# Optimization experiments

Hardware: AMD Instinct MI355X
Metric: run time of the kernel (lower is better)

The kernel has to match this reference:

```python
import jax, jax.numpy as jnp
import numpy as np

V, D, T, L, H = 32000, 1024, 2048, 2, 16
HS = D // H  # per-head dim (head_size // nheads)
FF = 4 * D
EPS = 1e-5


def _ln(x, g, b):
    m = jnp.mean(x, axis=-1, keepdims=True)
    v = jnp.mean((x - m) ** 2, axis=-1, keepdims=True)
    return (x - m) * jax.lax.rsqrt(v + EPS) * g + b


def setup_inputs() -> dict:
    key = jax.random.key(0)
    ks = jax.random.split(key, 16)
    s = lambda k, shape, fan: jax.random.normal(k, shape, jnp.float32) * (fan ** -0.5)
    return {
        "inputs": jax.random.randint(ks[0], (1, T), 0, V, dtype=jnp.int64),
        "tok_emb": s(ks[1], (V, D), D),
        "pos_emb": s(ks[2], (T, D), D),
        "ln1_g": jnp.ones((L, D)), "ln1_b": jnp.zeros((L, D)),
        "wq": s(ks[3], (L, H, D, HS), D),
        "wk": s(ks[4], (L, H, D, HS), D),
        "wv": s(ks[5], (L, H, D, HS), D),
        "ln2_g": jnp.ones((L, D)), "ln2_b": jnp.zeros((L, D)),
        "w1": s(ks[6], (L, D, FF), D), "b1": jnp.zeros((L, FF)),
        "w2": s(ks[7], (L, FF, D), FF), "b2": jnp.zeros((L, D)),
        "lnf_g": jnp.ones((D,)), "lnf_b": jnp.zeros((D,)),
        "w_un": s(ks[8], (D, V), D), "b_un": jnp.zeros((V,)),
    }


def reference(inputs, tok_emb, pos_emb, ln1_g, ln1_b, wq, wk, wv,
              ln2_g, ln2_b, w1, b1, w2, b2, lnf_g, lnf_b, w_un, b_un):
    b, t = inputs.shape
    x = tok_emb[inputs] + pos_emb[:t]  # [B,T,D]
    mask = jnp.tril(jnp.ones((t, t), dtype=bool))
    scale = jnp.asarray(D, x.dtype) ** -0.5  # source scales by x.shape[-1]**-0.5
    neg_inf = jnp.asarray(-jnp.inf, x.dtype)
    for l in range(L):
        h = _ln(x, ln1_g[l], ln1_b[l])
        q = jnp.einsum('btc,hcs->bhts', h, wq[l])
        k = jnp.einsum('btc,hcs->bhts', h, wk[l])
        v = jnp.einsum('btc,hcs->bhts', h, wv[l])
        scores = jnp.einsum('bhts,bhus->bhtu', q, k) * scale  # [B,H,T,T]
        scores = jnp.where(mask, scores, neg_inf)
        p = jax.nn.softmax(scores, axis=-1)
        att = jnp.einsum('bhtu,bhus->bhts', p, v)  # [B,H,T,HS]
        att = att.transpose(0, 2, 1, 3).reshape(b, t, H * HS)
        x = x + att
        h = _ln(x, ln2_g[l], ln2_b[l])
        h = jax.nn.relu(h @ w1[l] + b1[l]) @ w2[l] + b2[l]
        x = x + h
    x = _ln(x, lnf_g, lnf_b)
    return x @ w_un + b_un  # [B,T,V]
```

## Files before the change

### kernel.cpp

```cpp
#include <hip/hip_runtime.h>
#include <hip/hip_bf16.h>

#define TT 2048
#define DD 1024
#define NH 16
#define HSZ 64
#define FFD 4096
#define VV 32000
#define NL 2

typedef __bf16 bf16x8 __attribute__((ext_vector_type(8)));
typedef float f32x4 __attribute__((ext_vector_type(4)));

__device__ __forceinline__ unsigned short f2bf(float f) {
    unsigned int u = __float_as_uint(f);
    return (unsigned short)((u + 0x7FFFu + ((u >> 16) & 1u)) >> 16);
}

#define GLL(gsrc, ldst) \
  __builtin_amdgcn_global_load_lds((const __attribute__((address_space(1))) void*)(gsrc), \
                                   (__attribute__((address_space(3))) void*)(ldst), 16, 0, 0)

#define SWZ64(L)  ((L) ^ ((((L) >> 7) & 3) << 4))
#define SWZ128(L) ((L) ^ ((((L) >> 7) & 7) << 4))

__global__ __launch_bounds__(256) void embed_kernel(
    const int* __restrict__ idx, const float* __restrict__ tok,
    const float* __restrict__ pos, float* __restrict__ x)
{
    int t = blockIdx.x;
    int d4 = threadIdx.x * 4;
    int token = idx[t];
    float4 a = *(const float4*)&tok[(size_t)token * DD + d4];
    float4 p = *(const float4*)&pos[(size_t)t * DD + d4];
    float4 r;
    r.x = a.x + p.x; r.y = a.y + p.y; r.z = a.z + p.z; r.w = a.w + p.w;
    *(float4*)&x[(size_t)t * DD + d4] = r;
}

__global__ __launch_bounds__(256) void ln_kernel(
    const float* __restrict__ x, const float* __restrict__ g,
    const float* __restrict__ b, unsigned short* __restrict__ out)
{
    int t = blockIdx.x;
    int tid = threadIdx.x;
    int d4 = tid * 4;
    float4 xv = *(const float4*)&x[(size_t)t * DD + d4];
    float s  = xv.x + xv.y + xv.z + xv.w;
    float s2 = xv.x*xv.x + xv.y*xv.y + xv.z*xv.z + xv.w*xv.w;
    #pragma unroll
    for (int off = 32; off >= 1; off >>= 1) {
        s  += __shfl_xor(s,  off);
        s2 += __shfl_xor(s2, off);
    }
    __shared__ float ls[4], ls2[4];
    int w = tid >> 6;
    if ((tid & 63) == 0) { ls[w] = s; ls2[w] = s2; }
    __syncthreads();
    float sum  = ls[0] + ls[1] + ls[2] + ls[3];
    float sum2 = ls2[0] + ls2[1] + ls2[2] + ls2[3];
    float mean = sum * (1.0f / DD);
    float var  = sum2 * (1.0f / DD) - mean * mean;
    float r = rsqrtf(var + 1e-5f);
    float4 gv = *(const float4*)&g[d4];
    float4 bv = *(const float4*)&b[d4];
    ushort4 pk;
    pk.x = f2bf((xv.x - mean) * r * gv.x + bv.x);
    pk.y = f2bf((xv.y - mean) * r * gv.y + bv.y);
    pk.z = f2bf((xv.z - mean) * r * gv.z + bv.z);
    pk.w = f2bf((xv.w - mean) * r * gv.w + bv.w);
    *(ushort4*)&out[(size_t)t * DD + d4] = pk;
}

__global__ __launch_bounds__(256) void tcast(
    const float* __restrict__ src, unsigned short* __restrict__ dst,
    int R, int C, size_t sstride, size_t dstride)
{
    __shared__ float tile[64][65];
    const float* s = src + (size_t)blockIdx.z * sstride;
    unsigned short* d = dst + (size_t)blockIdx.z * dstride;
    int c0 = blockIdx.x * 64, r0 = blockIdx.y * 64;
    #pragma unroll
    for (int i = 0; i < 16; ++i) {
        int id = i * 256 + threadIdx.x;
        int rr = id >> 6, cc = id & 63;
        tile[rr][cc] = s[(size_t)(r0 + rr) * C + (c0 + cc)];
    }
    __syncthreads();
    #pragma unroll
    for (int i = 0; i < 16; ++i) {
        int id = i * 256 + threadIdx.x;
        int cc = id >> 6, rr = id & 63;
        d[(size_t)(c0 + cc) * R + (r0 + rr)] = f2bf(tile[rr][cc]);
    }
}

__global__ __launch_bounds__(256) void qkv_tcast(
    const float* __restrict__ wq, const float* __restrict__ wk,
    const float* __restrict__ wv, unsigned short* __restrict__ dst)
{
    __shared__ float tile[64][65];
    int l = blockIdx.z;
    int mat = blockIdx.y >> 4, hh = blockIdx.y & 15;
    const float* s = (mat == 0) ? wq : (mat == 1) ? wk : wv;
    s += (((size_t)l * NH + hh) * DD) * HSZ;
    int r0 = blockIdx.x * 64;
    #pragma unroll
    for (int i = 0; i < 16; ++i) {
        int id = i * 256 + threadIdx.x;
        int rr = id >> 6, cc = id & 63;
        tile[rr][cc] = s[(size_t)(r0 + rr) * HSZ + cc];
    }
    __syncthreads();
    unsigned short* d = dst + (size_t)l * 3072 * DD + ((size_t)mat * DD + hh * HSZ) * DD;
    #pragma unroll
    for (int i = 0; i < 16; ++i) {
        int id = i * 256 + threadIdx.x;
        int cc = id >> 6, rr = id & 63;
        d[(size_t)cc * DD + (r0 + rr)] = f2bf(tile[rr][cc]);
    }
}

template<int EPI>
__global__ __launch_bounds__(256) void mgemm(
    const unsigned short* __restrict__ A, const unsigned short* __restrict__ Bt,
    const float* __restrict__ bias, void* __restrict__ outp,
    int M, int N, int K)
{
    __shared__ unsigned short As[2][128 * 32];
    __shared__ unsigned short Bs[2][128 * 32];
    int tid = threadIdx.x;
    int w = tid >> 6, lane = tid & 63;
    int l15 = lane & 15, l4 = lane >> 4;
    int bm = blockIdx.y * 128, bn = blockIdx.x * 128;
    int wr = (w >> 1) * 64, wc = (w & 1) * 64;

    f32x4 zz = {0.f, 0.f, 0.f, 0.f};
    f32x4 acc[4][4];
    #pragma unroll
    for (int m = 0; m < 4; ++m)
        #pragma unroll
        for (int n = 0; n < 4; ++n) acc[m][n] = zz;

    int t16 = tid * 16;
    int lg = SWZ64(t16);
    int srow = lg >> 6;
    int skel = (lg & 63) >> 1;
    const unsigned short* aS0 = A + (size_t)(bm + srow) * K + skel;
    const unsigned short* aS1 = A + (size_t)(bm + 64 + srow) * K + skel;
    const unsigned short* bS0 = Bt + (size_t)(bn + srow) * K + skel;
    const unsigned short* bS1 = Bt + (size_t)(bn + 64 + srow) * K + skel;

    #define STAGE(t, buf) do { int kk_ = (t) * 32; \
        GLL(aS0 + kk_, (char*)As[buf] + w * 1024); \
        GLL(aS1 + kk_, (char*)As[buf] + 4096 + w * 1024); \
        GLL(bS0 + kk_, (char*)Bs[buf] + w * 1024); \
        GLL(bS1 + kk_, (char*)Bs[buf] + 4096 + w * 1024); } while (0)

    int aoff[4], boff[4];
    #pragma unroll
    for (int m = 0; m < 4; ++m) {
        int la = (wr + m * 16 + l15) * 64 + l4 * 16;
        aoff[m] = SWZ64(la);
        int lb = (wc + m * 16 + l15) * 64 + l4 * 16;
        boff[m] = SWZ64(lb);
    }

    int nt = K >> 5;
    STAGE(0, 0);
    STAGE(1, 1);
    for (int t = 0; t < nt; ++t) {
        int buf = t & 1;
        if (t + 1 < nt) asm volatile("s_waitcnt vmcnt(4)" ::: "memory");
        else            asm volatile("s_waitcnt vmcnt(0)" ::: "memory");
        __builtin_amdgcn_sched_barrier(0);
        __builtin_amdgcn_s_barrier();
        __builtin_amdgcn_sched_barrier(0);
        bf16x8 af[4], bfr[4];
        #pragma unroll
        for (int m = 0; m < 4; ++m) af[m] = *(const bf16x8*)((const char*)As[buf] + aoff[m]);
        #pragma unroll
        for (int n = 0; n < 4; ++n) bfr[n] = *(const bf16x8*)((const char*)Bs[buf] + boff[n]);
        #pragma unroll
        for (int m = 0; m < 4; ++m)
            #pragma unroll
            for (int n = 0; n < 4; ++n)
                acc[m][n] = __builtin_amdgcn_mfma_f32_16x16x32_bf16(af[m], bfr[n], acc[m][n], 0, 0, 0);
        __builtin_amdgcn_sched_barrier(0);
        __builtin_amdgcn_s_barrier();
        __builtin_amdgcn_sched_barrier(0);
        if (t + 2 < nt) STAGE(t + 2, buf);
    }
    #undef STAGE

    #pragma unroll
    for (int m = 0; m < 4; ++m) {
        int row0 = bm + wr + m * 16 + l4 * 4;
        #pragma unroll
        for (int n = 0; n < 4; ++n) {
            int col = bn + wc + n * 16 + l15;
            f32x4 v = acc[m][n];
            if (EPI == 0) {
                int mat = col >> 10, hh = (col >> 6) & 15, ss = col & 63;
                unsigned short* base = (unsigned short*)outp + (size_t)mat * ((size_t)NH * TT * HSZ);
                if (mat < 2) {
                    #pragma unroll
                    for (int i = 0; i < 4; ++i)
                        base[((size_t)hh * TT + row0 + i) * HSZ + ss] = f2bf(v[i]);
                } else {
                    ushort4 pk;
                    pk.x = f2bf(v[0]); pk.y = f2bf(v[1]); pk.z = f2bf(v[2]); pk.w = f2bf(v[3]);
                    *(ushort4*)&base[((size_t)hh * HSZ + ss) * TT + row0] = pk;
                }
            } else if (EPI == 1) {
                float bb = bias[col];
                unsigned short* o = (unsigned short*)outp;
                #pragma unroll
                for (int i = 0; i < 4; ++i)
                    o[(size_t)(row0 + i) * FFD + col] = f2bf(fmaxf(v[i] + bb, 0.f));
            } else if (EPI == 2) {
                float bb = bias[col];
                float* xx = (float*)outp;
                #pragma unroll
                for (int i = 0; i < 4; ++i)
                    xx[(size_t)(row0 + i) * DD + col] += v[i] + bb;
            }
        }
    }
}

__global__ __launch_bounds__(512, 2) void mgemm256(
    const unsigned short* __restrict__ A, const unsigned short* __restrict__ Bt,
    const float* __restrict__ bias, float* __restrict__ outp,
    int M, int N, int K)
{
    __shared__ unsigned short As[2][2][128 * 64];
    __shared__ unsigned short Bs[2][2][128 * 64];
    int tid = threadIdx.x;
    int w = tid >> 6, lane = tid & 63;
    int l15 = lane & 15, l4 = lane >> 4;
    int wr = w >> 2, wc = w & 3;
    int bid = blockIdx.x;
    int xcd = bid & 7, j = bid >> 3;
    int mt = j & 7, p = xcd * 16 + (j >> 3);
    if (p >= N / 256) return;
    int bm = mt * 256, bn = p * 256;

    f32x4 zz = {0.f, 0.f, 0.f, 0.f};
    f32x4 acc[8][4];
    #pragma unroll
    for (int m = 0; m < 8; ++m)
        #pragma unroll
        for (int n = 0; n < 4; ++n) acc[m][n] = zz;

    int L0 = w * 1024 + lane * 16;
    int Ls = SWZ128(L0);
    int srow = Ls >> 7;
    int skel = (Ls & 127) >> 1;
    const unsigned short* aS[2], *bS[2];
    aS[0] = A + (size_t)(bm + srow) * K + skel;
    aS[1] = A + (size_t)(bm + 128 + srow) * K + skel;
    bS[0] = Bt + (size_t)(bn + srow) * K + skel;
    bS[1] = Bt + (size_t)(bn + 128 + srow) * K + skel;
    size_t g1 = (size_t)64 * K;

    #define STAGE6(t, buf) do { int kk_ = (t) * 64; \
        GLL(aS[0] + kk_,      (char*)As[buf][0] + w * 1024); \
        GLL(aS[0] + g1 + kk_, (char*)As[buf][0] + 8192 + w * 1024); \
        GLL(aS[1] + kk_,      (char*)As[buf][1] + w * 1024); \
        GLL(aS[1] + g1 + kk_, (char*)As[buf][1] + 8192 + w * 1024); \
        GLL(bS[0] + kk_,      (char*)Bs[buf][0] + w * 1024); \
        GLL(bS[0] + g1 + kk_, (char*)Bs[buf][0] + 8192 + w * 1024); \
        GLL(bS[1] + kk_,      (char*)Bs[buf][1] + w * 1024); \
        GLL(bS[1] + g1 + kk_, (char*)Bs[buf][1] + 8192 + w * 1024); } while (0)

    int aoff[8][2], boff[4][2];
    #pragma unroll
    for (int m = 0; m < 8; ++m)
        #pragma unroll
        for (int ks = 0; ks < 2; ++ks) {
            int La = (m * 16 + l15) * 128 + ks * 64 + l4 * 16;
            aoff[m][ks] = SWZ128(La);
        }
    #pragma unroll
    for (int n = 0; n < 4; ++n)
        #pragma unroll
        for (int ks = 0; ks < 2; ++ks) {
            int Lb = ((wc & 1) * 64 + n * 16 + l15) * 128 + ks * 64 + l4 * 16;
            boff[n][ks] = SWZ128(Lb);
        }

    int nt = K >> 6;
    STAGE6(0, 0);
    STAGE6(1, 1);
    for (int t = 0; t < nt; ++t) {
        int buf = t & 1;
        if (t + 1 < nt) asm volatile("s_waitcnt vmcnt(8)" ::: "memory");
        else            asm volatile("s_waitcnt vmcnt(0)" ::: "memory");
        __builtin_amdgcn_sched_barrier(0);
        __builtin_amdgcn_s_barrier();
        __builtin_amdgcn_sched_barrier(0);
        const char* ab = (const char*)As[buf][wr];
        const char* bb = (const char*)Bs[buf][wc >> 1];
        bf16x8 bfr[4][2];
        #pragma unroll
        for (int n = 0; n < 4; ++n)
            #pragma unroll
            for (int ks = 0; ks < 2; ++ks)
                bfr[n][ks] = *(const bf16x8*)(bb + boff[n][ks]);
        __builtin_amdgcn_s_setprio(1);
        #pragma unroll
        for (int rh = 0; rh < 2; ++rh) {
            bf16x8 af[4][2];
            #pragma unroll
            for (int mm = 0; mm < 4; ++mm)
                #pragma unroll
                for (int ks = 0; ks < 2; ++ks)
                    af[mm][ks] = *(const bf16x8*)(ab + aoff[rh * 4 + mm][ks]);
            #pragma unroll
            for (int mm = 0; mm < 4; ++mm)
                #pragma unroll
                for (int n = 0; n < 4; ++n) {
                    acc[rh*4+mm][n] = __builtin_amdgcn_mfma_f32_16x16x32_bf16(af[mm][0], bfr[n][0], acc[rh*4+mm][n], 0, 0, 0);
                    acc[rh*4+mm][n] = __builtin_amdgcn_mfma_f32_16x16x32_bf16(af[mm][1], bfr[n][1], acc[rh*4+mm][n], 0, 0, 0);
                }
        }
        __builtin_amdgcn_s_setprio(0);
        __builtin_amdgcn_sched_barrier(0);
        __builtin_amdgcn_s_barrier();
        __builtin_amdgcn_sched_barrier(0);
        if (t + 2 < nt) STAGE6(t + 2, buf);
    }
    #undef STAGE6

    #pragma unroll
    for (int m = 0; m < 8; ++m) {
        int row0 = bm + wr * 128 + m * 16 + l4 * 4;
        #pragma unroll
        for (int n = 0; n < 4; ++n) {
            int col = bn + wc * 64 + n * 16 + l15;
            float bb = bias[col];
            f32x4 v = acc[m][n];
            #pragma unroll
            for (int i = 0; i < 4; ++i)
                outp[(size_t)(row0 + i) * VV + col] = v[i] + bb;
        }
    }
}

__global__ __launch_bounds__(256) void attn_kernel(
    const unsigned short* __restrict__ qg, const unsigned short* __restrict__ kg,
    const unsigned short* __restrict__ vt, float* __restrict__ x)
{
    __shared__ unsigned short Ks[2][64 * 64];
    __shared__ unsigned short Vs[2][64 * 64];
    __shared__ unsigned short Ps[4][16 * 64];
    int tid = threadIdx.x;
    int w = tid >> 6, lane = tid & 63;
    int l15 = lane & 15, l4 = lane >> 4;
    int hh = blockIdx.y;
    int qb = blockIdx.x * 64;

    const unsigned short* qrow = qg + ((size_t)hh * TT + qb + w * 16 + l15) * HSZ + l4 * 8;
    bf16x8 qf0 = *(const bf16x8*)(qrow);
    bf16x8 qf1 = *(const bf16x8*)(qrow + 32);

    int t16 = tid * 16;
    int lgs = SWZ128(t16);
    int surow = lgs >> 7;
    int subyte = lgs & 127;
    const char* kbase = (const char*)(kg + (size_t)hh * TT * HSZ);
    const char* vbase = (const char*)(vt + (size_t)hh * HSZ * TT);

    #define ASTAGE(ib, buf) do { \
        int ub_ = (ib) * 64; \
        GLL(kbase + (size_t)(ub_ + surow) * 128 + subyte,          (char*)Ks[buf] + w * 1024); \
        GLL(kbase + (size_t)(ub_ + 32 + surow) * 128 + subyte,     (char*)Ks[buf] + 4096 + w * 1024); \
        GLL(vbase + (size_t)surow * 4096 + ub_ * 2 + subyte,       (char*)Vs[buf] + w * 1024); \
        GLL(vbase + (size_t)(surow + 32) * 4096 + ub_ * 2 + subyte,(char*)Vs[buf] + 4096 + w * 1024); \
    } while (0)

    f32x4 zz = {0.f, 0.f, 0.f, 0.f};
    f32x4 o[4];
    #pragma unroll
    for (int i = 0; i < 4; ++i) o[i] = zz;
    float mrun = -INFINITY, lrun = 0.f;

    const float scale = 0.03125f;
    int nkv = (qb >> 6) + 1;
    ASTAGE(0, 0);
    __syncthreads();
    int cur = 0;
    for (int ib = 0; ib < nkv; ++ib) {
        int ub = ib * 64;
        bool diag = (ub == qb);
        if (ib + 1 < nkv) ASTAGE(ib + 1, cur ^ 1);
        const char* ksc = (const char*)Ks[cur];
        const char* vsc = (const char*)Vs[cur];

        f32x4 sfr[4];
        __builtin_amdgcn_s_setprio(1);
        #pragma unroll
        for (int f = 0; f < 4; ++f) {
            int lgb = (f * 16 + l15) * 128 + l4 * 16;
            bf16x8 k0 = *(const bf16x8*)(ksc + SWZ128(lgb));
            bf16x8 k1 = *(const bf16x8*)(ksc + SWZ128(lgb + 64));
            f32x4 z = zz;
            z = __builtin_amdgcn_mfma_f32_16x16x32_bf16(k0, qf0, z, 0, 0, 0);
            z = __builtin_amdgcn_mfma_f32_16x16x32_bf16(k1, qf1, z, 0, 0, 0);
            sfr[f] = z;
        }
        __builtin_amdgcn_s_setprio(0);

        float mx = -INFINITY;
        #pragma unroll
        for (int f = 0; f < 4; ++f)
            #pragma unroll
            for (int i = 0; i < 4; ++i) {
                float s = sfr[f][i] * scale;
                if (diag && (16 * f + (l4 << 2) + i) > (w * 16 + l15)) s = -INFINITY;
                sfr[f][i] = s;
                mx = fmaxf(mx, s);
            }
        mx = fmaxf(mx, __shfl_xor(mx, 16));
        mx = fmaxf(mx, __shfl_xor(mx, 32));
        float mn = fmaxf(mrun, mx);
        float c = __expf(mrun - mn);
        mrun = mn;
        float ps = 0.f;
        #pragma unroll
        for (int f = 0; f < 4; ++f)
            #pragma unroll
            for (int i = 0; i < 4; ++i) {
                float p = __expf(sfr[f][i] - mn);
                sfr[f][i] = p;
                ps += p;
            }
        ps += __shfl_xor(ps, 16);
        ps += __shfl_xor(ps, 32);
        lrun = lrun * c + ps;
        #pragma unroll
        for (int i = 0; i < 4; ++i) {
            float ci = __shfl(c, (lane & 48) + (l4 << 2) + i);
            #pragma unroll
            for (int sf = 0; sf < 4; ++sf) o[sf][i] *= ci;
        }

        unsigned short* pw = Ps[w];
        #pragma unroll
        for (int f = 0; f < 4; ++f) {
            unsigned a0 = ((unsigned)f2bf(sfr[f][0])) | (((unsigned)f2bf(sfr[f][1])) << 16);
            unsigned a1 = ((unsigned)f2bf(sfr[f][2])) | (((unsigned)f2bf(sfr[f][3])) << 16);
            int byte0 = l15 * 128 + (16 * f + (l4 << 2)) * 2;
            *(unsigned*)((char*)pw + SWZ128(byte0)) = a0;
            *(unsigned*)((char*)pw + SWZ128(byte0 + 4)) = a1;
        }
        bf16x8 pa0 = *(const bf16x8*)((const char*)pw + SWZ128(l15 * 128 + l4 * 16));
        bf16x8 pa1 = *(const bf16x8*)((const char*)pw + SWZ128(l15 * 128 + 64 + l4 * 16));
        __builtin_amdgcn_s_setprio(1);
        #pragma unroll
        for (int sf = 0; sf < 4; ++sf) {
            int lgb = (sf * 16 + l15) * 128 + l4 * 16;
            bf16x8 v0 = *(const bf16x8*)(vsc + SWZ128(lgb));
            bf16x8 v1 = *(const bf16x8*)(vsc + SWZ128(lgb + 64));
            o[sf] = __builtin_amdgcn_mfma_f32_16x16x32_bf16(pa0, v0, o[sf], 0, 0, 0);
            o[sf] = __builtin_amdgcn_mfma_f32_16x16x32_bf16(pa1, v1, o[sf], 0, 0, 0);
        }
        __builtin_amdgcn_s_setprio(0);
        __syncthreads();
        cur ^= 1;
    }
    #undef ASTAGE
    float rl[4];
    #pragma unroll
    for (int i = 0; i < 4; ++i)
        rl[i] = 1.0f / __shfl(lrun, (lane & 48) + (l4 << 2) + i);
    #pragma unroll
    for (int sf = 0; sf < 4; ++sf)
        #pragma unroll
        for (int i = 0; i < 4; ++i) {
            int q = qb + w * 16 + l4 * 4 + i;
            int d = hh * HSZ + sf * 16 + l15;
            x[(size_t)q * DD + d] += o[sf][i] * rl[i];
        }
}

extern "C" void kernel_launch(void* const* d_in, const int* in_sizes, int n_in,
                              void* d_out, int out_size, void* d_ws, size_t ws_size,
                              hipStream_t stream)
{
    const int*   idx    = (const int*)  d_in[0];
    const float* tok    = (const float*)d_in[1];
    const float* pos    = (const float*)d_in[2];
    const float* ln1_g  = (const float*)d_in[3];
    const float* ln1_b  = (const float*)d_in[4];
    const float* wq     = (const float*)d_in[5];
    const float* wk     = (const float*)d_in[6];
    const float* wv     = (const float*)d_in[7];
    const float* ln2_g  = (const float*)d_in[8];
    const float* ln2_b  = (const float*)d_in[9];
    const float* w1     = (const float*)d_in[10];
    const float* b1     = (const float*)d_in[11];
    const float* w2     = (const float*)d_in[12];
    const float* b2     = (const float*)d_in[13];
    const float* lnf_g  = (const float*)d_in[14];
    const float* lnf_b  = (const float*)d_in[15];
    const float* w_un   = (const float*)d_in[16];
    const float* b_un   = (const float*)d_in[17];
    float* out = (float*)d_out;

    char* W = (char*)d_ws;
    float*          x    = (float*)(W);
    unsigned short* h    = (unsigned short*)(W + 8388608);
    unsigned short* qg   = (unsigned short*)(W + 12582912);
    unsigned short* kg   = (unsigned short*)(W + 16777216);
    unsigned short* vt   = (unsigned short*)(W + 20971520);
    unsigned short* h1   = (unsigned short*)(W + 25165824);
    unsigned short* wqkvT= (unsigned short*)(W + 41943040);
    unsigned short* w1T  = (unsigned short*)(W + 54525952);
    unsigned short* w2T  = (unsigned short*)(W + 71303168);
    unsigned short* wunT = (unsigned short*)(W + 88080384);
    (void)kg; (void)ws_size; (void)in_sizes; (void)n_in; (void)out_size;

    qkv_tcast<<<dim3(16, 48, 2), 256, 0, stream>>>(wq, wk, wv, wqkvT);
    tcast<<<dim3(64, 16, 2), 256, 0, stream>>>(w1, w1T, DD, FFD, (size_t)DD * FFD, (size_t)DD * FFD);
    tcast<<<dim3(16, 64, 2), 256, 0, stream>>>(w2, w2T, FFD, DD, (size_t)FFD * DD, (size_t)FFD * DD);
    tcast<<<dim3(500, 16, 1), 256, 0, stream>>>(w_un, wunT, DD, VV, 0, 0);

    embed_kernel<<<TT, 256, 0, stream>>>(idx, tok, pos, x);

    for (int l = 0; l < NL; ++l) {
        ln_kernel<<<TT, 256, 0, stream>>>(x, ln1_g + l * DD, ln1_b + l * DD, h);
        mgemm<0><<<dim3(24, 16), 256, 0, stream>>>(h, wqkvT + (size_t)l * 3072 * DD, nullptr, qg, TT, 3072, DD);
        attn_kernel<<<dim3(32, 16), 256, 0, stream>>>(qg, kg, vt, x);
        ln_kernel<<<TT, 256, 0, stream>>>(x, ln2_g + l * DD, ln2_b + l * DD, h);
        mgemm<1><<<dim3(32, 16), 256, 0, stream>>>(h, w1T + (size_t)l * FFD * DD, b1 + (size_t)l * FFD, h1, TT, FFD, DD);
        mgemm<2><<<dim3(8, 16), 256, 0, stream>>>(h1, w2T + (size_t)l * DD * FFD, b2 + (size_t)l * DD, x, TT, DD, FFD);
    }

    ln_kernel<<<TT, 256, 0, stream>>>(x, lnf_g, lnf_b, h);
    mgemm256<<<dim3(1024), 512, 0, stream>>>(h, wunT, b_un, out, TT, VV, DD);
}
```

Measured before the change: 702.2 us.

## Triple-buffer GEMM loads, prefetch attention KV deeper, add lazy softmax rescale

Result: slower. 717.7 us (+2.2%).

```diff
diff --git a/kernel.cpp b/kernel.cpp
--- a/kernel.cpp
+++ b/kernel.cpp
@@ -127,8 +127,8 @@
     const float* __restrict__ bias, void* __restrict__ outp,
     int M, int N, int K)
 {
-    __shared__ unsigned short As[2][128 * 32];
-    __shared__ unsigned short Bs[2][128 * 32];
+    __shared__ unsigned short As[3][128 * 32];
+    __shared__ unsigned short Bs[3][128 * 32];
     int tid = threadIdx.x;
     int w = tid >> 6, lane = tid & 63;
     int l15 = lane & 15, l4 = lane >> 4;
@@ -151,11 +151,11 @@
     const unsigned short* bS0 = Bt + (size_t)(bn + srow) * K + skel;
     const unsigned short* bS1 = Bt + (size_t)(bn + 64 + srow) * K + skel;
 
-    #define STAGE(t, buf) do { int kk_ = (t) * 32; \
-        GLL(aS0 + kk_, (char*)As[buf] + w * 1024); \
-        GLL(aS1 + kk_, (char*)As[buf] + 4096 + w * 1024); \
-        GLL(bS0 + kk_, (char*)Bs[buf] + w * 1024); \
-        GLL(bS1 + kk_, (char*)Bs[buf] + 4096 + w * 1024); } while (0)
+    #define STAGE(t, slot) do { int kk_ = (t) * 32; \
+        GLL(aS0 + kk_, (char*)As[slot] + w * 1024); \
+        GLL(aS1 + kk_, (char*)As[slot] + 4096 + w * 1024); \
+        GLL(bS0 + kk_, (char*)Bs[slot] + w * 1024); \
+        GLL(bS1 + kk_, (char*)Bs[slot] + 4096 + w * 1024); } while (0)
 
     int aoff[4], boff[4];
     #pragma unroll
@@ -169,18 +169,20 @@
     int nt = K >> 5;
     STAGE(0, 0);
     STAGE(1, 1);
+    STAGE(2, 2);
+    int slot = 0;
     for (int t = 0; t < nt; ++t) {
-        int buf = t & 1;
-        if (t + 1 < nt) asm volatile("s_waitcnt vmcnt(4)" ::: "memory");
-        else            asm volatile("s_waitcnt vmcnt(0)" ::: "memory");
+        if (t + 2 < nt)      asm volatile("s_waitcnt vmcnt(8)" ::: "memory");
+        else if (t + 1 < nt) asm volatile("s_waitcnt vmcnt(4)" ::: "memory");
+        else                 asm volatile("s_waitcnt vmcnt(0)" ::: "memory");
         __builtin_amdgcn_sched_barrier(0);
         __builtin_amdgcn_s_barrier();
         __builtin_amdgcn_sched_barrier(0);
         bf16x8 af[4], bfr[4];
         #pragma unroll
-        for (int m = 0; m < 4; ++m) af[m] = *(const bf16x8*)((const char*)As[buf] + aoff[m]);
-        #pragma unroll
-        for (int n = 0; n < 4; ++n) bfr[n] = *(const bf16x8*)((const char*)Bs[buf] + boff[n]);
+        for (int m = 0; m < 4; ++m) af[m] = *(const bf16x8*)((const char*)As[slot] + aoff[m]);
+        #pragma unroll
+        for (int n = 0; n < 4; ++n) bfr[n] = *(const bf16x8*)((const char*)Bs[slot] + boff[n]);
         #pragma unroll
         for (int m = 0; m < 4; ++m)
             #pragma unroll
@@ -189,7 +191,8 @@
         __builtin_amdgcn_sched_barrier(0);
         __builtin_amdgcn_s_barrier();
         __builtin_amdgcn_sched_barrier(0);
-        if (t + 2 < nt) STAGE(t + 2, buf);
+        if (t + 3 < nt) STAGE(t + 3, slot);
+        slot = (slot == 2) ? 0 : slot + 1;
     }
     #undef STAGE
 
@@ -234,8 +237,8 @@
     const float* __restrict__ bias, float* __restrict__ outp,
     int M, int N, int K)
 {
-    __shared__ unsigned short As[2][2][128 * 64];
-    __shared__ unsigned short Bs[2][2][128 * 64];
+    __shared__ unsigned short As[3][2][128 * 32];
+    __shared__ unsigned short Bs[3][2][128 * 32];
     int tid = threadIdx.x;
     int w = tid >> 6, lane = tid & 63;
     int l15 = lane & 15, l4 = lane >> 4;
@@ -253,83 +256,61 @@
         #pragma unroll
         for (int n = 0; n < 4; ++n) acc[m][n] = zz;
 
-    int L0 = w * 1024 + lane * 16;
-    int Ls = SWZ128(L0);
-    int srow = Ls >> 7;
-    int skel = (Ls & 127) >> 1;
+    int L0 = tid * 16;
+    int Ls = SWZ64(L0);
+    int srow = Ls >> 6;
+    int skel = (Ls & 63) >> 1;
     const unsigned short* aS[2], *bS[2];
     aS[0] = A + (size_t)(bm + srow) * K + skel;
     aS[1] = A + (size_t)(bm + 128 + srow) * K + skel;
     bS[0] = Bt + (size_t)(bn + srow) * K + skel;
     bS[1] = Bt + (size_t)(bn + 128 + srow) * K + skel;
-    size_t g1 = (size_t)64 * K;
-
-    #define STAGE6(t, buf) do { int kk_ = (t) * 64; \
-        GLL(aS[0] + kk_,      (char*)As[buf][0] + w * 1024); \
-        GLL(aS[0] + g1 + kk_, (char*)As[buf][0] + 8192 + w * 1024); \
-        GLL(aS[1] + kk_,      (char*)As[buf][1] + w * 1024); \
-        GLL(aS[1] + g1 + kk_, (char*)As[buf][1] + 8192 + w * 1024); \
-        GLL(bS[0] + kk_,      (char*)Bs[buf][0] + w * 1024); \
-        GLL(bS[0] + g1 + kk_, (char*)Bs[buf][0] + 8192 + w * 1024); \
-        GLL(bS[1] + kk_,      (char*)Bs[buf][1] + w * 1024); \
-        GLL(bS[1] + g1 + kk_, (char*)Bs[buf][1] + 8192 + w * 1024); } while (0)
-
-    int aoff[8][2], boff[4][2];
+
+    #define STAGE6(t, slot) do { int kk_ = (t) * 32; \
+        GLL(aS[0] + kk_, (char*)As[slot][0] + w * 1024); \
+        GLL(aS[1] + kk_, (char*)As[slot][1] + w * 1024); \
+        GLL(bS[0] + kk_, (char*)Bs[slot][0] + w * 1024); \
+        GLL(bS[1] + kk_, (char*)Bs[slot][1] + w * 1024); } while (0)
+
+    int aoff[8], boff[4];
     #pragma unroll
     for (int m = 0; m < 8; ++m)
-        #pragma unroll
-        for (int ks = 0; ks < 2; ++ks) {
-            int La = (m * 16 + l15) * 128 + ks * 64 + l4 * 16;
-            aoff[m][ks] = SWZ128(La);
-        }
+        aoff[m] = SWZ64((m * 16 + l15) * 64 + l4 * 16);
     #pragma unroll
     for (int n = 0; n < 4; ++n)
-        #pragma unroll
-        for (int ks = 0; ks < 2; ++ks) {
-            int Lb = ((wc & 1) * 64 + n * 16 + l15) * 128 + ks * 64 + l4 * 16;
-            boff[n][ks] = SWZ128(Lb);
-        }
-
-    int nt = K >> 6;
+        boff[n] = SWZ64(((wc & 1) * 64 + n * 16 + l15) * 64 + l4 * 16);
+
+    int nt = K >> 5;
     STAGE6(0, 0);
     STAGE6(1, 1);
+    STAGE6(2, 2);
+    int slot = 0;
     for (int t = 0; t < nt; ++t) {
-        int buf = t & 1;
-        if (t + 1 < nt) asm volatile("s_waitcnt vmcnt(8)" ::: "memory");
-        else            asm volatile("s_waitcnt vmcnt(0)" ::: "memory");
+        if (t + 2 < nt)      asm volatile("s_waitcnt vmcnt(8)" ::: "memory");
+        else if (t + 1 < nt) asm volatile("s_waitcnt vmcnt(4)" ::: "memory");
+        else                 asm volatile("s_waitcnt vmcnt(0)" ::: "memory");
         __builtin_amdgcn_sched_barrier(0);
         __builtin_amdgcn_s_barrier();
         __builtin_amdgcn_sched_barrier(0);
-        const char* ab = (const char*)As[buf][wr];
-        const char* bb = (const char*)Bs[buf][wc >> 1];
-        bf16x8 bfr[4][2];
-        #pragma unroll
-        for (int n = 0; n < 4; ++n)
+        const char* ab = (const char*)As[slot][wr];
+        const char* bb = (const char*)Bs[slot][wc >> 1];
+        bf16x8 bfr[4];
+        #pragma unroll
+        for (int n = 0; n < 4; ++n) bfr[n] = *(const bf16x8*)(bb + boff[n]);
+        __builtin_amdgcn_s_setprio(1);
+        #pragma unroll
+        for (int m = 0; m < 8; ++m) {
+            bf16x8 af = *(const bf16x8*)(ab + aoff[m]);
             #pragma unroll
-            for (int ks = 0; ks < 2; ++ks)
-                bfr[n][ks] = *(const bf16x8*)(bb + boff[n][ks]);
-        __builtin_amdgcn_s_setprio(1);
-        #pragma unroll
-        for (int rh = 0; rh < 2; ++rh) {
-            bf16x8 af[4][2];
-            #pragma unroll
-            for (int mm = 0; mm < 4; ++mm)
-                #pragma unroll
-                for (int ks = 0; ks < 2; ++ks)
-                    af[mm][ks] = *(const bf16x8*)(ab + aoff[rh * 4 + mm][ks]);
-            #pragma unroll
-            for (int mm = 0; mm < 4; ++mm)
-                #pragma unroll
-                for (int n = 0; n < 4; ++n) {
-                    acc[rh*4+mm][n] = __builtin_amdgcn_mfma_f32_16x16x32_bf16(af[mm][0], bfr[n][0], acc[rh*4+mm][n], 0, 0, 0);
-                    acc[rh*4+mm][n] = __builtin_amdgcn_mfma_f32_16x16x32_bf16(af[mm][1], bfr[n][1], acc[rh*4+mm][n], 0, 0, 0);
-                }
+            for (int n = 0; n < 4; ++n)
+                acc[m][n] = __builtin_amdgcn_mfma_f32_16x16x32_bf16(af, bfr[n], acc[m][n], 0, 0, 0);
         }
         __builtin_amdgcn_s_setprio(0);
         __builtin_amdgcn_sched_barrier(0);
         __builtin_amdgcn_s_barrier();
         __builtin_amdgcn_sched_barrier(0);
-        if (t + 2 < nt) STAGE6(t + 2, buf);
+        if (t + 3 < nt) STAGE6(t + 3, slot);
+        slot = (slot == 2) ? 0 : slot + 1;
     }
     #undef STAGE6
 
@@ -359,7 +340,7 @@
     int w = tid >> 6, lane = tid & 63;
     int l15 = lane & 15, l4 = lane >> 4;
     int hh = blockIdx.y;
-    int qb = blockIdx.x * 64;
+    int qb = (31 - blockIdx.x) * 64;
 
     const unsigned short* qrow = qg + ((size_t)hh * TT + qb + w * 16 + l15) * HSZ + l4 * 8;
     bf16x8 qf0 = *(const bf16x8*)(qrow);
@@ -389,12 +370,15 @@
     const float scale = 0.03125f;
     int nkv = (qb >> 6) + 1;
     ASTAGE(0, 0);
-    __syncthreads();
+    if (nkv > 1) ASTAGE(1, 1);
     int cur = 0;
     for (int ib = 0; ib < nkv; ++ib) {
-        int ub = ib * 64;
-        bool diag = (ub == qb);
-        if (ib + 1 < nkv) ASTAGE(ib + 1, cur ^ 1);
+        bool diag = (ib * 64 == qb);
+        if (ib + 1 < nkv) asm volatile("s_waitcnt vmcnt(4)" ::: "memory");
+        else              asm volatile("s_waitcnt vmcnt(0)" ::: "memory");
+        __builtin_amdgcn_sched_barrier(0);
+        __builtin_amdgcn_s_barrier();
+        __builtin_amdgcn_sched_barrier(0);
         const char* ksc = (const char*)Ks[cur];
         const char* vsc = (const char*)Vs[cur];
 
@@ -424,26 +408,32 @@
             }
         mx = fmaxf(mx, __shfl_xor(mx, 16));
         mx = fmaxf(mx, __shfl_xor(mx, 32));
-        float mn = fmaxf(mrun, mx);
-        float c = __expf(mrun - mn);
-        mrun = mn;
+        bool grow = __any(mx > mrun + 8.0f);
+        float c = 1.0f;
+        if (grow) {
+            float mn = fmaxf(mrun, mx);
+            c = __expf(mrun - mn);
+            mrun = mn;
+        }
         float ps = 0.f;
         #pragma unroll
         for (int f = 0; f < 4; ++f)
             #pragma unroll
             for (int i = 0; i < 4; ++i) {
-                float p = __expf(sfr[f][i] - mn);
+                float p = __expf(sfr[f][i] - mrun);
                 sfr[f][i] = p;
                 ps += p;
             }
         ps += __shfl_xor(ps, 16);
         ps += __shfl_xor(ps, 32);
         lrun = lrun * c + ps;
-        #pragma unroll
-        for (int i = 0; i < 4; ++i) {
-            float ci = __shfl(c, (lane & 48) + (l4 << 2) + i);
+        if (grow) {
             #pragma unroll
-            for (int sf = 0; sf < 4; ++sf) o[sf][i] *= ci;
+            for (int i = 0; i < 4; ++i) {
+                float ci = __shfl(c, (lane & 48) + (l4 << 2) + i);
+                #pragma unroll
+                for (int sf = 0; sf < 4; ++sf) o[sf][i] *= ci;
+            }
         }
 
         unsigned short* pw = Ps[w];
@@ -467,7 +457,10 @@
             o[sf] = __builtin_amdgcn_mfma_f32_16x16x32_bf16(pa1, v1, o[sf], 0, 0, 0);
         }
         __builtin_amdgcn_s_setprio(0);
-        __syncthreads();
+        __builtin_amdgcn_sched_barrier(0);
+        __builtin_amdgcn_s_barrier();
+        __builtin_amdgcn_sched_barrier(0);
+        if (ib + 2 < nkv) ASTAGE(ib + 2, cur);
         cur ^= 1;
     }
     #undef ASTAGE
```

## Triple-buffer GEMM, add BN=64 tiles, reverse attention order, lazy softmax rescale

Applied to the files above, without the earlier changes.

After: 658.9 us. -6.2%, faster.

```diff
diff --git a/kernel.cpp b/kernel.cpp
--- a/kernel.cpp
+++ b/kernel.cpp
@@ -23,6 +23,8 @@
 
 #define SWZ64(L)  ((L) ^ ((((L) >> 7) & 3) << 4))
 #define SWZ128(L) ((L) ^ ((((L) >> 7) & 7) << 4))
+
+#define VMW(n) asm volatile("s_waitcnt vmcnt(" #n ")" ::: "memory")
 
 __global__ __launch_bounds__(256) void embed_kernel(
     const int* __restrict__ idx, const float* __restrict__ tok,
@@ -121,26 +123,27 @@
     }
 }
 
-template<int EPI>
+template<int EPI, int BN>
 __global__ __launch_bounds__(256) void mgemm(
     const unsigned short* __restrict__ A, const unsigned short* __restrict__ Bt,
     const float* __restrict__ bias, void* __restrict__ outp,
     int M, int N, int K)
 {
-    __shared__ unsigned short As[2][128 * 32];
-    __shared__ unsigned short Bs[2][128 * 32];
+    constexpr int FN = BN / 64 * 2;
+    __shared__ unsigned short As[3][128 * 32];
+    __shared__ unsigned short Bs[3][BN * 32];
     int tid = threadIdx.x;
     int w = tid >> 6, lane = tid & 63;
     int l15 = lane & 15, l4 = lane >> 4;
-    int bm = blockIdx.y * 128, bn = blockIdx.x * 128;
-    int wr = (w >> 1) * 64, wc = (w & 1) * 64;
+    int bm = blockIdx.y * 128, bn = blockIdx.x * BN;
+    int wr = (w >> 1) * 64, wc = (w & 1) * (BN / 2);
 
     f32x4 zz = {0.f, 0.f, 0.f, 0.f};
-    f32x4 acc[4][4];
+    f32x4 acc[4][FN];
     #pragma unroll
     for (int m = 0; m < 4; ++m)
         #pragma unroll
-        for (int n = 0; n < 4; ++n) acc[m][n] = zz;
+        for (int n = 0; n < FN; ++n) acc[m][n] = zz;
 
     int t16 = tid * 16;
     int lg = SWZ64(t16);
@@ -151,45 +154,53 @@
     const unsigned short* bS0 = Bt + (size_t)(bn + srow) * K + skel;
     const unsigned short* bS1 = Bt + (size_t)(bn + 64 + srow) * K + skel;
 
-    #define STAGE(t, buf) do { int kk_ = (t) * 32; \
-        GLL(aS0 + kk_, (char*)As[buf] + w * 1024); \
-        GLL(aS1 + kk_, (char*)As[buf] + 4096 + w * 1024); \
-        GLL(bS0 + kk_, (char*)Bs[buf] + w * 1024); \
-        GLL(bS1 + kk_, (char*)Bs[buf] + 4096 + w * 1024); } while (0)
-
-    int aoff[4], boff[4];
-    #pragma unroll
-    for (int m = 0; m < 4; ++m) {
-        int la = (wr + m * 16 + l15) * 64 + l4 * 16;
-        aoff[m] = SWZ64(la);
-        int lb = (wc + m * 16 + l15) * 64 + l4 * 16;
-        boff[m] = SWZ64(lb);
-    }
+    #define STAGE(t, slot) do { int kk_ = (t) * 32; \
+        GLL(aS0 + kk_, (char*)As[slot] + w * 1024); \
+        GLL(aS1 + kk_, (char*)As[slot] + 4096 + w * 1024); \
+        GLL(bS0 + kk_, (char*)Bs[slot] + w * 1024); \
+        if (BN == 128) GLL(bS1 + kk_, (char*)Bs[slot] + 4096 + w * 1024); } while (0)
+
+    int aoff[4], boff[FN];
+    #pragma unroll
+    for (int m = 0; m < 4; ++m)
+        aoff[m] = SWZ64((wr + m * 16 + l15) * 64 + l4 * 16);
+    #pragma unroll
+    for (int n = 0; n < FN; ++n)
+        boff[n] = SWZ64((wc + n * 16 + l15) * 64 + l4 * 16);
 
     int nt = K >> 5;
     STAGE(0, 0);
     STAGE(1, 1);
+    STAGE(2, 2);
+    int slot = 0;
     for (int t = 0; t < nt; ++t) {
-        int buf = t & 1;
-        if (t + 1 < nt) asm volatile("s_waitcnt vmcnt(4)" ::: "memory");
-        else            asm volatile("s_waitcnt vmcnt(0)" ::: "memory");
+        if (BN == 128) {
+            if (t + 2 < nt)      VMW(8);
+            else if (t + 1 < nt) VMW(4);
+            else                 VMW(0);
+        } else {
+            if (t + 2 < nt)      VMW(6);
+            else if (t + 1 < nt) VMW(3);
+            else                 VMW(0);
+        }
         __builtin_amdgcn_sched_barrier(0);
         __builtin_amdgcn_s_barrier();
         __builtin_amdgcn_sched_barrier(0);
-        bf16x8 af[4], bfr[4];
-        #pragma unroll
-        for (int m = 0; m < 4; ++m) af[m] = *(const bf16x8*)((const char*)As[buf] + aoff[m]);
-        #pragma unroll
-        for (int n = 0; n < 4; ++n) bfr[n] = *(const bf16x8*)((const char*)Bs[buf] + boff[n]);
+        bf16x8 af[4], bfr[FN];
+        #pragma unroll
+        for (int m = 0; m < 4; ++m) af[m] = *(const bf16x8*)((const char*)As[slot] + aoff[m]);
+        #pragma unroll
+        for (int n = 0; n < FN; ++n) bfr[n] = *(const bf16x8*)((const char*)Bs[slot] + boff[n]);
         #pragma unroll
         for (int m = 0; m < 4; ++m)
             #pragma unroll
-            for (int n = 0; n < 4; ++n)
+            for (int n = 0; n < FN; ++n)
                 acc[m][n] = __builtin_amdgcn_mfma_f32_16x16x32_bf16(af[m], bfr[n], acc[m][n], 0, 0, 0);
         __builtin_amdgcn_sched_barrier(0);
         __builtin_amdgcn_s_barrier();
         __builtin_amdgcn_sched_barrier(0);
-        if (t + 2 < nt) STAGE(t + 2, buf);
+        if (t + 3 < nt) STAGE(t + 3, slot);
+        slot = (slot == 2) ? 0 : slot + 1;
     }
     #undef STAGE
 
@@ -197,7 +208,7 @@
     for (int m = 0; m < 4; ++m) {
         int row0 = bm + wr + m * 16 + l4 * 4;
         #pragma unroll
-        for (int n = 0; n < 4; ++n) {
+        for (int n = 0; n < FN; ++n) {
             int col = bn + wc + n * 16 + l15;
             f32x4 v = acc[m][n];
             if (EPI == 0) {
@@ -295,8 +306,8 @@
     STAGE6(1, 1);
     for (int t = 0; t < nt; ++t) {
         int buf = t & 1;
-        if (t + 1 < nt) asm volatile("s_waitcnt vmcnt(8)" ::: "memory");
-        else            asm volatile("s_waitcnt vmcnt(0)" ::: "memory");
+        if (t + 1 < nt) VMW(8);
+        else            VMW(0);
         __builtin_amdgcn_sched_barrier(0);
         __builtin_amdgcn_s_barrier();
         __builtin_amdgcn_sched_barrier(0);
@@ -359,7 +370,7 @@
     int w = tid >> 6, lane = tid & 63;
     int l15 = lane & 15, l4 = lane >> 4;
     int hh = blockIdx.y;
-    int qb = blockIdx.x * 64;
+    int qb = (31 - blockIdx.x) * 64;
 
     const unsigned short* qrow = qg + ((size_t)hh * TT + qb + w * 16 + l15) * HSZ + l4 * 8;
     bf16x8 qf0 = *(const bf16x8*)(qrow);
@@ -389,12 +400,15 @@
     const float scale = 0.03125f;
     int nkv = (qb >> 6) + 1;
     ASTAGE(0, 0);
-    __syncthreads();
+    if (nkv > 1) ASTAGE(1, 1);
     int cur = 0;
     for (int ib = 0; ib < nkv; ++ib) {
-        int ub = ib * 64;
-        bool diag = (ub == qb);
-        if (ib + 1 < nkv) ASTAGE(ib + 1, cur ^ 1);
+        bool diag = (ib * 64 == qb);
+        if (ib + 1 < nkv) VMW(4);
+        else              VMW(0);
+        __builtin_amdgcn_sched_barrier(0);
+        __builtin_amdgcn_s_barrier();
+        __builtin_amdgcn_sched_barrier(0);
         const char* ksc = (const char*)Ks[cur];
         const char* vsc = (const char*)Vs[cur];
 
@@ -424,26 +438,32 @@
             }
         mx = fmaxf(mx, __shfl_xor(mx, 16));
         mx = fmaxf(mx, __shfl_xor(mx, 32));
-        float mn = fmaxf(mrun, mx);
-        float c = __expf(mrun - mn);
-        mrun = mn;
+        bool grow = __any(mx > mrun + 8.0f);
+        float c = 1.0f;
+        if (grow) {
+            float mn = fmaxf(mrun, mx);
+            c = __expf(mrun - mn);
+            mrun = mn;
+        }
         float ps = 0.f;
         #pragma unroll
         for (int f = 0; f < 4; ++f)
             #pragma unroll
             for (int i = 0; i < 4; ++i) {
-                float p = __expf(sfr[f][i] - mn);
+                float p = __expf(sfr[f][i] - mrun);
                 sfr[f][i] = p;
                 ps += p;
             }
         ps += __shfl_xor(ps, 16);
         ps += __shfl_xor(ps, 32);
         lrun = lrun * c + ps;
-        #pragma unroll
-        for (int i = 0; i < 4; ++i) {
-            float ci = __shfl(c, (lane & 48) + (l4 << 2) + i);
-            #pragma unroll
-            for (int sf = 0; sf < 4; ++sf) o[sf][i] *= ci;
+        if (grow) {
+            #pragma unroll
+            for (int i = 0; i < 4; ++i) {
+                float ci = __shfl(c, (lane & 48) + (l4 << 2) + i);
+                #pragma unroll
+                for (int sf = 0; sf < 4; ++sf) o[sf][i] *= ci;
+            }
         }
 
         unsigned short* pw = Ps[w];
@@ -467,7 +487,10 @@
             o[sf] = __builtin_amdgcn_mfma_f32_16x16x32_bf16(pa1, v1, o[sf], 0, 0, 0);
         }
         __builtin_amdgcn_s_setprio(0);
-        __syncthreads();
+        __builtin_amdgcn_sched_barrier(0);
+        __builtin_amdgcn_s_barrier();
+        __builtin_amdgcn_sched_barrier(0);
+        if (ib + 2 < nkv) ASTAGE(ib + 2, cur);
         cur ^= 1;
     }
     #undef ASTAGE
@@ -531,11 +554,11 @@
 
     for (int l = 0; l < NL; ++l) {
         ln_kernel<<<TT, 256, 0, stream>>>(x, ln1_g + l * DD, ln1_b + l * DD, h);
-        mgemm<0><<<dim3(24, 16), 256, 0, stream>>>(h, wqkvT + (size_t)l * 3072 * DD, nullptr, qg, TT, 3072, DD);
+        mgemm<0, 64><<<dim3(48, 16), 256, 0, stream>>>(h, wqkvT + (size_t)l * 3072 * DD, nullptr, qg, TT, 3072, DD);
         attn_kernel<<<dim3(32, 16), 256, 0, stream>>>(qg, kg, vt, x);
         ln_kernel<<<TT, 256, 0, stream>>>(x, ln2_g + l * DD, ln2_b + l * DD, h);
-        mgemm<1><<<dim3(32, 16), 256, 0, stream>>>(h, w1T + (size_t)l * FFD * DD, b1 + (size_t)l * FFD, h1, TT, FFD, DD);
-        mgemm<2><<<dim3(8, 16), 256, 0, stream>>>(h1, w2T + (size_t)l * DD * FFD, b2 + (size_t)l * DD, x, TT, DD, FFD);
+        mgemm<1, 128><<<dim3(32, 16), 256, 0, stream>>>(h, w1T + (size_t)l * FFD * DD, b1 + (size_t)l * FFD, h1, TT, FFD, DD);
+        mgemm<2, 64><<<dim3(16, 16), 256, 0, stream>>>(h1, w2T + (size_t)l * DD * FFD, b2 + (size_t)l * DD, x, TT, DD, FFD);
     }
 
     ln_kernel<<<TT, 256, 0, stream>>>(x, lnf_g, lnf_b, h);
```
